# Optimization experiments

Measured on AMD Instinct MI355X. Metric: run time of the kernel, lower is better.

The kernel has to match this reference:

```python
import jax, jax.numpy as jnp
import numpy as np

N = 100000   # nodes
E = 400000   # edges
G = 2048     # graphs in batch
H = 128      # hidden_channels
V = 100      # in_channels (element vocab)
L = 3        # hidden_layers (GAT)
LO = 2       # out_layers (dense)
SLOPE = 0.2  # GATConv negative_slope default


def setup_inputs() -> dict:
    key = jax.random.key(0)
    ks = jax.random.split(key, 14)
    s = 1.0 / np.sqrt(H)
    return {
        "x": jax.random.randint(ks[0], (N,), 0, V),
        "edge_index": jax.random.randint(ks[1], (2, E), 0, N),
        "edge_attr": jax.random.uniform(ks[2], (E, 1), dtype=jnp.float32),
        "batch": jnp.sort(jax.random.randint(ks[3], (N,), 0, G)),
        "emb": jax.random.normal(ks[4], (V, H), dtype=jnp.float32),
        "gat_W": jax.random.normal(ks[5], (L, H, H), dtype=jnp.float32) * s,
        "att_src": jax.random.normal(ks[6], (L, H), dtype=jnp.float32) * s,
        "att_dst": jax.random.normal(ks[7], (L, H), dtype=jnp.float32) * s,
        "edge_W": jax.random.normal(ks[8], (L, H), dtype=jnp.float32) * s,  # lin_edge: Linear(1, H, bias=False)
        "att_edge": jax.random.normal(ks[9], (L, H), dtype=jnp.float32) * s,
        "gat_b": jnp.zeros((L, H), dtype=jnp.float32),
        "lin_W": jax.random.normal(ks[10], (LO, H, H), dtype=jnp.float32) * s,
        "lin_b": jnp.zeros((LO, H), dtype=jnp.float32),
        "wp_W": jax.random.normal(ks[11], (H, 1), dtype=jnp.float32) * s,
        "wp_b": jnp.zeros((1,), dtype=jnp.float32),
    }


def _segment_softmax(logits, seg, num_segments):
    m = jax.ops.segment_max(logits, seg, num_segments=num_segments)
    e = jnp.exp(logits - m[seg])
    s = jax.ops.segment_sum(e, seg, num_segments=num_segments)
    return e / s[seg]


def reference(x, edge_index, edge_attr, batch, emb, gat_W, att_src, att_dst,
              edge_W, att_edge, gat_b, lin_W, lin_b, wp_W, wp_b):
    src, dst = edge_index[0], edge_index[1]
    # GATConv add_self_loops=True with fill_value='mean' for edge_attr
    loop = jnp.arange(N, dtype=src.dtype)
    src_sl = jnp.concatenate([src, loop])          # [E+N]
    dst_sl = jnp.concatenate([dst, loop])          # [E+N]
    ea_mean = jnp.mean(edge_attr, axis=0, keepdims=True)  # [1,1]
    ea_sl = jnp.concatenate([edge_attr, jnp.broadcast_to(ea_mean, (N, 1))], axis=0)  # [E+N,1]

    h = emb[x]  # [N,H]
    for l in range(L):
        xt = h @ gat_W[l]                 # shared lin_src/lin_dst, heads=1
        a_s = xt @ att_src[l]             # [N]
        a_d = xt @ att_dst[l]             # [N]
        a_e = (ea_sl * edge_W[l][None, :]) @ att_edge[l]  # lin_edge then att_edge: [E+N]
        alpha = jax.nn.leaky_relu(a_s[src_sl] + a_d[dst_sl] + a_e, negative_slope=SLOPE)
        alpha = _segment_softmax(alpha, dst_sl, N)
        out = jax.ops.segment_sum(xt[src_sl] * alpha[:, None], dst_sl, num_segments=N)
        out = out + gat_b[l]
        # F.normalize(h_x, 2, dim=1)
        nrm = jnp.linalg.norm(out, axis=1, keepdims=True)
        h = out / jnp.maximum(nrm, 1e-12)
    for i in range(LO):
        h = jax.nn.relu(h @ lin_W[i] + lin_b[i])
    m_x = jax.ops.segment_sum(h, batch, num_segments=G)  # scatter_sum readout [G,H]
    props = m_x @ wp_W + wp_b                            # [G,1]
    return jnp.squeeze(props, axis=1)                    # [G]
```

## Files before the change

### kernel.cpp

```cpp
#include <hip/hip_runtime.h>
#include <math.h>

#define N_NODES 100000
#define N_EDGES 400000
#define NG 2048
#define H 128
#define NV 100
#define NLAYERS 3
#define SLOPE 0.2f

#define SCAL_N 64

typedef __attribute__((ext_vector_type(8))) short bf16x8;
typedef __attribute__((ext_vector_type(4))) float f32x4;

__device__ __forceinline__ float wave_reduce_sum(float v){
  #pragma unroll
  for (int off = 32; off > 0; off >>= 1) v += __shfl_xor(v, off, 64);
  return v;
}
__device__ __forceinline__ unsigned short rne_bf16(float f){
  unsigned int u = __float_as_uint(f);
  u += 0x7FFF + ((u >> 16) & 1);
  return (unsigned short)(u >> 16);
}
__device__ __forceinline__ unsigned int pack_bf16x2(float lo, float hi){
  return ((unsigned int)rne_bf16(hi) << 16) | rne_bf16(lo);
}

#define PB_CONVW 320
#define PB_CONVE (PB_CONVW + 50)
#define PB_OUT   (PB_CONVE + 8)
#define PB_DOTS  (PB_OUT + 1)
#define PB_EASUM (PB_DOTS + 256)
#define PB_DEG   (PB_EASUM + 1954)
__global__ __launch_bounds__(256) void k_prep(
    const float* __restrict__ gat_W, const float* __restrict__ lin_W,
    unsigned short* __restrict__ Wf,
    const float* __restrict__ emb, unsigned short* __restrict__ embb,
    const float* __restrict__ ea, const float* __restrict__ ew,
    const float* __restrict__ ae, float* __restrict__ scal,
    const float* __restrict__ wp_b, float* __restrict__ out,
    const int* __restrict__ ei, int* __restrict__ deg,
    int* __restrict__ rank)
{
  int b = blockIdx.x, tid = threadIdx.x;
  if (b < PB_CONVW){
    int i = b*256 + tid;
    int m   = i >> 14;
    int r   = i & 16383;
    int k0i = r >> 12;
    int r3  = r & 4095;
    int ct  = r3 >> 9;
    int r4  = r3 & 511;
    int lane= r4 >> 3;
    int j   = r4 & 7;
    int q = lane >> 4, ln = lane & 15;
    int k = k0i*32 + q*8 + j;
    int n = ct*16 + ln;
    const float* src = (m < 3) ? (gat_W + m*16384) : (lin_W + (m-3)*16384);
    Wf[i] = rne_bf16(src[k*H + n]);
  } else if (b < PB_CONVE){
    int i = (b - PB_CONVW)*256 + tid;
    if (i < NV*H) embb[i] = rne_bf16(emb[i]);
  } else if (b < PB_OUT){
    int g = (b - PB_CONVE)*256 + tid;
    if (g < NG) out[g] = wp_b[0];
  } else if (b < PB_DOTS){
    int l = tid >> 6, ln = tid & 63;
    if (l < NLAYERS){
      float p = ew[l*H + ln]*ae[l*H + ln] + ew[l*H + ln + 64]*ae[l*H + ln + 64];
      p = wave_reduce_sum(p);
      if (ln == 0) atomicAdd(&scal[32 + l], p);
    }
  } else if (b < PB_EASUM){
    int i = (b - PB_DOTS)*256 + tid;
    int stride = 256*256;
    float v = 0.f;
    for (; i < N_EDGES; i += stride) v += ea[i];
    v = wave_reduce_sum(v);
    if ((tid & 63) == 0) atomicAdd(&scal[0], v);
  } else {
    int i = (b - PB_EASUM)*256 + tid;
    if (i < N_EDGES + N_NODES){
      int d = (i < N_EDGES) ? ei[N_EDGES + i] : (i - N_EDGES);
      rank[i] = atomicAdd(&deg[d], 1);
    }
  }
}

__global__ __launch_bounds__(256) void k_alloc(
    const int* __restrict__ deg, int* __restrict__ row_ptr, int* __restrict__ counter){
  __shared__ int wsum[4];
  __shared__ int base;
  int n = blockIdx.x * 256 + threadIdx.x;
  int d = (n < N_NODES) ? deg[n] : 0;
  int lane = threadIdx.x & 63, wid = threadIdx.x >> 6;
  int v = d;
  #pragma unroll
  for (int off = 1; off < 64; off <<= 1){
    int u = __shfl_up(v, off, 64);
    if (lane >= off) v += u;
  }
  if (lane == 63) wsum[wid] = v;
  __syncthreads();
  if (threadIdx.x == 0){
    int t0 = wsum[0], t1 = wsum[1], t2 = wsum[2], t3 = wsum[3];
    base = atomicAdd(counter, t0 + t1 + t2 + t3);
    wsum[0] = 0; wsum[1] = t0; wsum[2] = t0 + t1; wsum[3] = t0 + t1 + t2;
  }
  __syncthreads();
  if (n < N_NODES) row_ptr[n] = base + wsum[wid] + (v - d);
}

__global__ void k_scatter(const int* __restrict__ ei, const float* __restrict__ ea,
                          const float* __restrict__ scal, const int* __restrict__ row_ptr,
                          const int* __restrict__ rank, int* __restrict__ csr_src,
                          float* __restrict__ csr_ea){
  int i = blockIdx.x * blockDim.x + threadIdx.x;
  if (i >= N_EDGES + N_NODES) return;
  int s, d; float v;
  if (i < N_EDGES){ s = ei[i]; d = ei[N_EDGES + i]; v = ea[i]; }
  else            { s = d = i - N_EDGES; v = scal[0] * (1.0f / N_EDGES); }
  int pos = row_ptr[d] + rank[i];
  csr_src[pos] = s;
  csr_ea[pos]  = v;
}

__global__ __launch_bounds__(256, 4) void k_gemm(
    const unsigned short* __restrict__ Ab, const int* __restrict__ xmap,
    const unsigned short* __restrict__ Wf,
    unsigned short* __restrict__ Cb,
    const float* __restrict__ att1, const float* __restrict__ att2,
    float* __restrict__ a_s_out, float* __restrict__ a_d_out)
{
  __shared__ unsigned short lw[16384];
  int tid  = threadIdx.x;
  int w    = tid >> 6;
  int lane = tid & 63;
  int q    = lane >> 4;
  int ln   = lane & 15;
  int waveRow = blockIdx.x*128 + w*32;

  #pragma unroll
  for (int i = 0; i < 8; ++i){
    int base = (i*256 + w*64) * 8;
    __builtin_amdgcn_global_load_lds(
        (const __attribute__((address_space(1))) unsigned int*)(Wf + base + lane*8),
        (__attribute__((address_space(3))) unsigned int*)(lw + base),
        16, 0, 0);
  }

  bf16x8 af[2][4];
  #pragma unroll
  for (int m = 0; m < 2; ++m){
    int r = waveRow + m*16 + ln;
    if (r >= N_NODES) r = N_NODES - 1;
    if (xmap) r = xmap[r];
    const unsigned short* Ar = Ab + (size_t)r*H;
    #pragma unroll
    for (int k0i = 0; k0i < 4; ++k0i)
      af[m][k0i] = *(const bf16x8*)(Ar + k0i*32 + q*8);
  }
  __syncthreads();

  f32x4 acc[2][8];
  #pragma unroll
  for (int m = 0; m < 2; ++m)
    #pragma unroll
    for (int ct = 0; ct < 8; ++ct) acc[m][ct] = (f32x4){0.f,0.f,0.f,0.f};

  #pragma unroll
  for (int k0i = 0; k0i < 4; ++k0i){
    #pragma unroll
    for (int ct = 0; ct < 8; ++ct){
      bf16x8 bw = *(const bf16x8*)(lw + k0i*4096 + ct*512 + lane*8);
      #pragma unroll
      for (int m = 0; m < 2; ++m)
        acc[m][ct] = __builtin_amdgcn_mfma_f32_16x16x32_bf16(af[m][k0i], bw, acc[m][ct], 0,0,0);
    }
  }

  float as_l[8], ad_l[8];
  #pragma unroll
  for (int ct = 0; ct < 8; ++ct){ as_l[ct] = att1[ct*16+ln]; ad_l[ct] = att2[ct*16+ln]; }
  #pragma unroll
  for (int m = 0; m < 2; ++m){
    #pragma unroll
    for (int r = 0; r < 4; ++r){
      int grow = waveRow + m*16 + q*4 + r;
      bool ok = grow < N_NODES;
      float ps = 0.f, pd = 0.f;
      #pragma unroll
      for (int ct = 0; ct < 8; ++ct){
        float v = acc[m][ct][r];
        if (ok) Cb[(size_t)grow*H + ct*16 + ln] = rne_bf16(v);
        ps += v * as_l[ct]; pd += v * ad_l[ct];
      }
      #pragma unroll
      for (int mk = 8; mk > 0; mk >>= 1){
        ps += __shfl_xor(ps, mk, 64);
        pd += __shfl_xor(pd, mk, 64);
      }
      if (ok && ln == 0){ a_s_out[grow] = ps; a_d_out[grow] = pd; }
    }
  }
}

__global__ __launch_bounds__(256, 4) void k_dense(
    const unsigned short* __restrict__ Ab,
    const unsigned short* __restrict__ Wf,
    const float* __restrict__ b1, const float* __restrict__ b2,
    const float* __restrict__ wp, const int* __restrict__ batch,
    float* __restrict__ out)
{
  __shared__ unsigned short lw[16384];
  int tid  = threadIdx.x;
  int w    = tid >> 6;
  int lane = tid & 63;
  int q    = lane >> 4;
  int ln   = lane & 15;
  int waveRow = blockIdx.x*128 + w*32;

  #pragma unroll
  for (int i = 0; i < 8; ++i){
    int base = (i*256 + w*64) * 8;
    __builtin_amdgcn_global_load_lds(
        (const __attribute__((address_space(1))) unsigned int*)(Wf + base + lane*8),
        (__attribute__((address_space(3))) unsigned int*)(lw + base),
        16, 0, 0);
  }
  bf16x8 af[2][4];
  #pragma unroll
  for (int m = 0; m < 2; ++m){
    int r = waveRow + m*16 + ln;
    if (r >= N_NODES) r = N_NODES - 1;
    const unsigned short* Ar = Ab + (size_t)r*H;
    #pragma unroll
    for (int k0i = 0; k0i < 4; ++k0i)
      af[m][k0i] = *(const bf16x8*)(Ar + k0i*32 + q*8);
  }
  __syncthreads();

  f32x4 acc[2][8];
  #pragma unroll
  for (int m = 0; m < 2; ++m)
    #pragma unroll
    for (int ct = 0; ct < 8; ++ct) acc[m][ct] = (f32x4){0.f,0.f,0.f,0.f};
  #pragma unroll
  for (int k0i = 0; k0i < 4; ++k0i){
    #pragma unroll
    for (int ct = 0; ct < 8; ++ct){
      bf16x8 bw = *(const bf16x8*)(lw + k0i*4096 + ct*512 + lane*8);
      #pragma unroll
      for (int m = 0; m < 2; ++m)
        acc[m][ct] = __builtin_amdgcn_mfma_f32_16x16x32_bf16(af[m][k0i], bw, acc[m][ct], 0,0,0);
    }
  }
  __syncthreads();

  unsigned short* lh = lw + (w << 12);
  float b1_l[8];
  #pragma unroll
  for (int ct = 0; ct < 8; ++ct) b1_l[ct] = b1[ct*16+ln];
  #pragma unroll
  for (int m = 0; m < 2; ++m){
    #pragma unroll
    for (int r = 0; r < 4; ++r){
      int lr = m*16 + q*4 + r;
      int sw = (lr & 7) << 3;
      #pragma unroll
      for (int ct = 0; ct < 8; ++ct){
        int col = ct*16 + ln;
        lh[lr*128 + (col ^ sw)] = rne_bf16(fmaxf(acc[m][ct][r] + b1_l[ct], 0.f));
      }
    }
  }
  __syncthreads();

  bf16x8 af2[2][4];
  #pragma unroll
  for (int m = 0; m < 2; ++m){
    int lr = m*16 + ln;
    int sw = (lr & 7) << 3;
    #pragma unroll
    for (int k0i = 0; k0i < 4; ++k0i)
      af2[m][k0i] = *(const bf16x8*)(lh + lr*128 + ((k0i*32 + q*8) ^ sw));
  }
  __syncthreads();

  #pragma unroll
  for (int i = 0; i < 8; ++i){
    int base = (i*256 + w*64) * 8;
    __builtin_amdgcn_global_load_lds(
        (const __attribute__((address_space(1))) unsigned int*)(Wf + 16384 + base + lane*8),
        (__attribute__((address_space(3))) unsigned int*)(lw + base),
        16, 0, 0);
  }
  __syncthreads();

  #pragma unroll
  for (int m = 0; m < 2; ++m)
    #pragma unroll
    for (int ct = 0; ct < 8; ++ct) acc[m][ct] = (f32x4){0.f,0.f,0.f,0.f};
  #pragma unroll
  for (int k0i = 0; k0i < 4; ++k0i){
    #pragma unroll
    for (int ct = 0; ct < 8; ++ct){
      bf16x8 bw = *(const bf16x8*)(lw + k0i*4096 + ct*512 + lane*8);
      #pragma unroll
      for (int m = 0; m < 2; ++m)
        acc[m][ct] = __builtin_amdgcn_mfma_f32_16x16x32_bf16(af2[m][k0i], bw, acc[m][ct], 0,0,0);
    }
  }

  float b2_l[8], wp_l[8];
  #pragma unroll
  for (int ct = 0; ct < 8; ++ct){ b2_l[ct] = b2[ct*16+ln]; wp_l[ct] = wp[ct*16+ln]; }
  #pragma unroll
  for (int m = 0; m < 2; ++m){
    #pragma unroll
    for (int r = 0; r < 4; ++r){
      int grow = waveRow + m*16 + q*4 + r;
      bool ok = grow < N_NODES;
      float ps = 0.f;
      #pragma unroll
      for (int ct = 0; ct < 8; ++ct)
        ps += fmaxf(acc[m][ct][r] + b2_l[ct], 0.f) * wp_l[ct];
      #pragma unroll
      for (int mk = 8; mk > 0; mk >>= 1) ps += __shfl_xor(ps, mk, 64);
      if (ok && ln == 0) atomicAdd(&out[batch[grow]], ps);
    }
  }
}

__global__ __launch_bounds__(256, 4) void k_aggregate(
    const uint4* __restrict__ xtb4, const float* __restrict__ a_s,
    const float* __restrict__ a_d, const int* __restrict__ csr_src,
    const float* __restrict__ csr_ea, const int* __restrict__ row_ptr,
    const int* __restrict__ deg, const float* __restrict__ scal, int l,
    const float* __restrict__ bias, uint4* __restrict__ hb4)
{
  __shared__ int   ls_s[4][4][16];
  __shared__ float ls_w[4][4][16];
  int wid  = threadIdx.x >> 6;
  int lane = threadIdx.x & 63;
  int h    = lane >> 4;
  int c    = lane & 15;
  int n    = blockIdx.x*16 + wid*4 + h;
  int beg = row_ptr[n];
  int d   = deg[n];
  float adn = a_d[n];
  float dl  = scal[32 + l];
  int v = d;
  v = max(v, __shfl_xor(v, 16, 64));
  v = max(v, __shfl_xor(v, 32, 64));
  int maxd = v;

  float4 acA = make_float4(0.f,0.f,0.f,0.f);
  float4 acB = make_float4(0.f,0.f,0.f,0.f);
  float ss = 0.f;
  for (int base = 0; base < maxd; base += 16){
    int j = base + c;
    bool vld = (j < d);
    int s = 0; float eaj = 0.f;
    if (vld){
      int e = beg + j;
      s   = csr_src[e];
      eaj = csr_ea[e];
    }
    ls_s[wid][h][c] = s;

    int cnt = (min(16, maxd - base) + 7) & ~7;

    uint4 xv[8];
    #pragma unroll
    for (int u = 0; u < 8; ++u)
      xv[u] = xtb4[(size_t)ls_s[wid][h][u]*(H/8) + c];

    float wgt = 0.f;
    if (vld){
      float lg = a_s[s] + adn + dl*eaj;
      lg = (lg > 0.f) ? lg : SLOPE*lg;
      wgt = __expf(lg);
    }
    ls_w[wid][h][c] = wgt;

    for (int j0 = 0; j0 < cnt; j0 += 8){
      if (j0){
        #pragma unroll
        for (int u = 0; u < 8; ++u)
          xv[u] = xtb4[(size_t)ls_s[wid][h][j0 + u]*(H/8) + c];
      }
      float w8[8];
      #pragma unroll
      for (int u = 0; u < 8; ++u) w8[u] = ls_w[wid][h][j0 + u];
      #pragma unroll
      for (int u = 0; u < 8; ++u){
        float wg = w8[u];
        acA.x += wg * __uint_as_float(xv[u].x << 16);
        acA.y += wg * __uint_as_float(xv[u].x & 0xFFFF0000u);
        acA.z += wg * __uint_as_float(xv[u].y << 16);
        acA.w += wg * __uint_as_float(xv[u].y & 0xFFFF0000u);
        acB.x += wg * __uint_as_float(xv[u].z << 16);
        acB.y += wg * __uint_as_float(xv[u].z & 0xFFFF0000u);
        acB.z += wg * __uint_as_float(xv[u].w << 16);
        acB.w += wg * __uint_as_float(xv[u].w & 0xFFFF0000u);
        ss    += wg;
      }
    }
  }

  float4 bvA = *(const float4*)(bias + c*8);
  float4 bvB = *(const float4*)(bias + c*8 + 4);
  float inv = 1.0f / ss;
  acA.x = acA.x*inv + bvA.x;
  acA.y = acA.y*inv + bvA.y;
  acA.z = acA.z*inv + bvA.z;
  acA.w = acA.w*inv + bvA.w;
  acB.x = acB.x*inv + bvB.x;
  acB.y = acB.y*inv + bvB.y;
  acB.z = acB.z*inv + bvB.z;
  acB.w = acB.w*inv + bvB.w;
  float sq = acA.x*acA.x + acA.y*acA.y + acA.z*acA.z + acA.w*acA.w
           + acB.x*acB.x + acB.y*acB.y + acB.z*acB.z + acB.w*acB.w;
  #pragma unroll
  for (int off = 8; off > 0; off >>= 1) sq += __shfl_xor(sq, off, 64);
  float rn = 1.0f / fmaxf(sqrtf(sq), 1e-12f);
  uint4 o;
  o.x = pack_bf16x2(acA.x*rn, acA.y*rn);
  o.y = pack_bf16x2(acA.z*rn, acA.w*rn);
  o.z = pack_bf16x2(acB.x*rn, acB.y*rn);
  o.w = pack_bf16x2(acB.z*rn, acB.w*rn);
  hb4[(size_t)n*(H/8) + c] = o;
}

extern "C" void kernel_launch(void* const* d_in, const int* in_sizes, int n_in,
                              void* d_out, int out_size, void* d_ws, size_t ws_size,
                              hipStream_t stream) {
  const int*   x          = (const int*)  d_in[0];
  const int*   edge_index = (const int*)  d_in[1];
  const float* edge_attr  = (const float*)d_in[2];
  const int*   batch      = (const int*)  d_in[3];
  const float* emb        = (const float*)d_in[4];
  const float* gat_W      = (const float*)d_in[5];
  const float* att_src    = (const float*)d_in[6];
  const float* att_dst    = (const float*)d_in[7];
  const float* edge_W     = (const float*)d_in[8];
  const float* att_edge   = (const float*)d_in[9];
  const float* gat_b      = (const float*)d_in[10];
  const float* lin_W      = (const float*)d_in[11];
  const float* lin_b      = (const float*)d_in[12];
  const float* wp_W       = (const float*)d_in[13];
  const float* wp_b       = (const float*)d_in[14];
  float* out = (float*)d_out;

  unsigned short* hb  = (unsigned short*)d_ws;
  unsigned short* xtb = hb + (size_t)N_NODES*H;
  unsigned short* Wt  = xtb + (size_t)N_NODES*H;
  unsigned short* embb= Wt + 5*16384;
  float* a_s    = (float*)(embb + NV*H);
  float* a_d    = a_s + N_NODES;
  float* csr_ea = a_d + N_NODES;
  float* scal   = csr_ea + (N_EDGES + N_NODES);
  int*   deg    = (int*)(scal + SCAL_N);
  int*   rank   = deg + N_NODES;
  int*   row_ptr= rank + (N_EDGES + N_NODES);
  int*   csr_src= row_ptr + N_NODES;

  hipMemsetAsync(scal, 0, (size_t)(SCAL_N + N_NODES) * sizeof(float), stream);

  k_prep<<<PB_DEG, 256, 0, stream>>>(
      gat_W, lin_W, Wt, emb, embb, edge_attr, edge_W, att_edge, scal,
      wp_b, out, edge_index, deg, rank);
  k_alloc<<<(N_NODES + 255)/256, 256, 0, stream>>>(deg, row_ptr, (int*)&scal[48]);
  k_scatter<<<(N_EDGES + N_NODES + 255)/256, 256, 0, stream>>>(
      edge_index, edge_attr, scal, row_ptr, rank, csr_src, csr_ea);

  const int gemm_grid = (N_NODES + 127) / 128;
  for (int l = 0; l < NLAYERS; ++l){
    k_gemm<<<gemm_grid, 256, 0, stream>>>(
        (l == 0) ? embb : hb, (l == 0) ? x : nullptr,
        Wt + (size_t)l*16384, xtb,
        att_src + l*H, att_dst + l*H, a_s, a_d);
    k_aggregate<<<(N_NODES + 15)/16, 256, 0, stream>>>(
        (const uint4*)xtb, a_s, a_d, csr_src, csr_ea, row_ptr, deg,
        scal, l, gat_b + l*H, (uint4*)hb);
  }
  k_dense<<<gemm_grid, 256, 0, stream>>>(
      hb, Wt + (size_t)3*16384, lin_b, lin_b + H, wp_W, batch, out);
}
```

Baseline: 298.5 us.

## Precompute layer-0 transform on vocab table and replace LDS staging with shuffles

Layer 0 input is emb[x], so xt = emb[x] @ W equals (emb @ W)[x]. The code now computes the transform and attention scalars once for the 100-row vocabulary inside an extra block of k_alloc, then gathers them per node in extra blocks of k_scatter, skipping the first full-size GEMM launch. The aggregate kernel also drops its shared-memory staging of source indices and weights in favour of wave shuffles, and issues both 8-edge gather batches up front. This costs more registers in aggregate and adds a gather pass that writes the full xt array.

Result: no change. 302.4 us (+1.3%).

```diff
diff --git a/kernel.cpp b/kernel.cpp
--- a/kernel.cpp
+++ b/kernel.cpp
@@ -89,46 +89,141 @@
   }
 }
 
+#define NALLOC ((N_NODES + 255)/256)
 __global__ __launch_bounds__(256) void k_alloc(
-    const int* __restrict__ deg, int* __restrict__ row_ptr, int* __restrict__ counter){
+    const int* __restrict__ deg, int* __restrict__ row_ptr, int* __restrict__ counter,
+    const unsigned short* __restrict__ embb, const unsigned short* __restrict__ Wf,
+    unsigned short* __restrict__ xt0b, const float* __restrict__ att1,
+    const float* __restrict__ att2, float* __restrict__ tabS, float* __restrict__ tabD)
+{
+  __shared__ unsigned short lw[16384];
   __shared__ int wsum[4];
-  __shared__ int base;
-  int n = blockIdx.x * 256 + threadIdx.x;
-  int d = (n < N_NODES) ? deg[n] : 0;
-  int lane = threadIdx.x & 63, wid = threadIdx.x >> 6;
-  int v = d;
-  #pragma unroll
-  for (int off = 1; off < 64; off <<= 1){
-    int u = __shfl_up(v, off, 64);
-    if (lane >= off) v += u;
-  }
-  if (lane == 63) wsum[wid] = v;
+  __shared__ int base_s;
+  if (blockIdx.x < NALLOC){
+    int n = blockIdx.x * 256 + threadIdx.x;
+    int d = (n < N_NODES) ? deg[n] : 0;
+    int lane = threadIdx.x & 63, wid = threadIdx.x >> 6;
+    int v = d;
+    #pragma unroll
+    for (int off = 1; off < 64; off <<= 1){
+      int u = __shfl_up(v, off, 64);
+      if (lane >= off) v += u;
+    }
+    if (lane == 63) wsum[wid] = v;
+    __syncthreads();
+    if (threadIdx.x == 0){
+      int t0 = wsum[0], t1 = wsum[1], t2 = wsum[2], t3 = wsum[3];
+      base_s = atomicAdd(counter, t0 + t1 + t2 + t3);
+      wsum[0] = 0; wsum[1] = t0; wsum[2] = t0 + t1; wsum[3] = t0 + t1 + t2;
+    }
+    __syncthreads();
+    if (n < N_NODES) row_ptr[n] = base_s + wsum[wid] + (v - d);
+    return;
+  }
+
+  int tid  = threadIdx.x;
+  int w    = tid >> 6;
+  int lane = tid & 63;
+  int q    = lane >> 4;
+  int ln   = lane & 15;
+  int waveRow = w*32;
+
+  #pragma unroll
+  for (int i = 0; i < 8; ++i){
+    int base = (i*256 + w*64) * 8;
+    __builtin_amdgcn_global_load_lds(
+        (const __attribute__((address_space(1))) unsigned int*)(Wf + base + lane*8),
+        (__attribute__((address_space(3))) unsigned int*)(lw + base),
+        16, 0, 0);
+  }
+  bf16x8 af[2][4];
+  #pragma unroll
+  for (int m = 0; m < 2; ++m){
+    int r = waveRow + m*16 + ln;
+    if (r >= NV) r = NV - 1;
+    const unsigned short* Ar = embb + (size_t)r*H;
+    #pragma unroll
+    for (int k0i = 0; k0i < 4; ++k0i)
+      af[m][k0i] = *(const bf16x8*)(Ar + k0i*32 + q*8);
+  }
   __syncthreads();
-  if (threadIdx.x == 0){
-    int t0 = wsum[0], t1 = wsum[1], t2 = wsum[2], t3 = wsum[3];
-    base = atomicAdd(counter, t0 + t1 + t2 + t3);
-    wsum[0] = 0; wsum[1] = t0; wsum[2] = t0 + t1; wsum[3] = t0 + t1 + t2;
-  }
-  __syncthreads();
-  if (n < N_NODES) row_ptr[n] = base + wsum[wid] + (v - d);
-}
-
+
+  f32x4 acc[2][8];
+  #pragma unroll
+  for (int m = 0; m < 2; ++m)
+    #pragma unroll
+    for (int ct = 0; ct < 8; ++ct) acc[m][ct] = (f32x4){0.f,0.f,0.f,0.f};
+  #pragma unroll
+  for (int k0i = 0; k0i < 4; ++k0i){
+    #pragma unroll
+    for (int ct = 0; ct < 8; ++ct){
+      bf16x8 bw = *(const bf16x8*)(lw + k0i*4096 + ct*512 + lane*8);
+      #pragma unroll
+      for (int m = 0; m < 2; ++m)
+        acc[m][ct] = __builtin_amdgcn_mfma_f32_16x16x32_bf16(af[m][k0i], bw, acc[m][ct], 0,0,0);
+    }
+  }
+
+  float as_l[8], ad_l[8];
+  #pragma unroll
+  for (int ct = 0; ct < 8; ++ct){ as_l[ct] = att1[ct*16+ln]; ad_l[ct] = att2[ct*16+ln]; }
+  #pragma unroll
+  for (int m = 0; m < 2; ++m){
+    #pragma unroll
+    for (int r = 0; r < 4; ++r){
+      int grow = waveRow + m*16 + q*4 + r;
+      bool ok = grow < NV;
+      float ps = 0.f, pd = 0.f;
+      #pragma unroll
+      for (int ct = 0; ct < 8; ++ct){
+        float v = acc[m][ct][r];
+        if (ok) xt0b[(size_t)grow*H + ct*16 + ln] = rne_bf16(v);
+        ps += v * as_l[ct]; pd += v * ad_l[ct];
+      }
+      #pragma unroll
+      for (int mk = 8; mk > 0; mk >>= 1){
+        ps += __shfl_xor(ps, mk, 64);
+        pd += __shfl_xor(pd, mk, 64);
+      }
+      if (ok && ln == 0){ tabS[grow] = ps; tabD[grow] = pd; }
+    }
+  }
+}
+
+#define NSCAT ((N_EDGES + N_NODES + 255)/256)
 __global__ void k_scatter(const int* __restrict__ ei, const float* __restrict__ ea,
                           const float* __restrict__ scal, const int* __restrict__ row_ptr,
                           const int* __restrict__ rank, int* __restrict__ csr_src,
-                          float* __restrict__ csr_ea){
-  int i = blockIdx.x * blockDim.x + threadIdx.x;
-  if (i >= N_EDGES + N_NODES) return;
-  int s, d; float v;
-  if (i < N_EDGES){ s = ei[i]; d = ei[N_EDGES + i]; v = ea[i]; }
-  else            { s = d = i - N_EDGES; v = scal[0] * (1.0f / N_EDGES); }
-  int pos = row_ptr[d] + rank[i];
-  csr_src[pos] = s;
-  csr_ea[pos]  = v;
+                          float* __restrict__ csr_ea,
+                          const int* __restrict__ x, const uint4* __restrict__ xt0b4,
+                          const float* __restrict__ tabS, const float* __restrict__ tabD,
+                          uint4* __restrict__ xtb4, float* __restrict__ a_s,
+                          float* __restrict__ a_d){
+  int b = blockIdx.x;
+  if (b < NSCAT){
+    int i = b * 256 + threadIdx.x;
+    if (i >= N_EDGES + N_NODES) return;
+    int s, d; float v;
+    if (i < N_EDGES){ s = ei[i]; d = ei[N_EDGES + i]; v = ea[i]; }
+    else            { s = d = i - N_EDGES; v = scal[0] * (1.0f / N_EDGES); }
+    int pos = row_ptr[d] + rank[i];
+    csr_src[pos] = s;
+    csr_ea[pos]  = v;
+    return;
+  }
+  int gb = b - NSCAT;
+  int t  = threadIdx.x;
+  int n  = gb*16 + (t >> 4);
+  int c  = t & 15;
+  if (n >= N_NODES) return;
+  int v  = x[n];
+  xtb4[(size_t)n*(H/8) + c] = xt0b4[(size_t)v*(H/8) + c];
+  if (c == 0)      a_s[n] = tabS[v];
+  else if (c == 1) a_d[n] = tabD[v];
 }
 
 __global__ __launch_bounds__(256, 4) void k_gemm(
-    const unsigned short* __restrict__ Ab, const int* __restrict__ xmap,
+    const unsigned short* __restrict__ Ab,
     const unsigned short* __restrict__ Wf,
     unsigned short* __restrict__ Cb,
     const float* __restrict__ att1, const float* __restrict__ att2,
@@ -156,7 +251,6 @@
   for (int m = 0; m < 2; ++m){
     int r = waveRow + m*16 + ln;
     if (r >= N_NODES) r = N_NODES - 1;
-    if (xmap) r = xmap[r];
     const unsigned short* Ar = Ab + (size_t)r*H;
     #pragma unroll
     for (int k0i = 0; k0i < 4; ++k0i)
@@ -341,13 +435,12 @@
     const int* __restrict__ deg, const float* __restrict__ scal, int l,
     const float* __restrict__ bias, uint4* __restrict__ hb4)
 {
-  __shared__ int   ls_s[4][4][16];
-  __shared__ float ls_w[4][4][16];
-  int wid  = threadIdx.x >> 6;
   int lane = threadIdx.x & 63;
   int h    = lane >> 4;
   int c    = lane & 15;
+  int wid  = threadIdx.x >> 6;
   int n    = blockIdx.x*16 + wid*4 + h;
+  if (n >= N_NODES) return;
   int beg = row_ptr[n];
   int d   = deg[n];
   float adn = a_d[n];
@@ -356,6 +449,7 @@
   v = max(v, __shfl_xor(v, 16, 64));
   v = max(v, __shfl_xor(v, 32, 64));
   int maxd = v;
+  int hq = h << 4;
 
   float4 acA = make_float4(0.f,0.f,0.f,0.f);
   float4 acB = make_float4(0.f,0.f,0.f,0.f);
@@ -369,14 +463,22 @@
       s   = csr_src[e];
       eaj = csr_ea[e];
     }
-    ls_s[wid][h][c] = s;
-
     int cnt = (min(16, maxd - base) + 7) & ~7;
-
-    uint4 xv[8];
-    #pragma unroll
-    for (int u = 0; u < 8; ++u)
-      xv[u] = xtb4[(size_t)ls_s[wid][h][u]*(H/8) + c];
+    bool two = (cnt > 8);
+
+    uint4 xv0[8], xv1[8];
+    #pragma unroll
+    for (int u = 0; u < 8; ++u){
+      int su = __shfl(s, hq + u, 64);
+      xv0[u] = xtb4[(size_t)su*(H/8) + c];
+    }
+    if (two){
+      #pragma unroll
+      for (int u = 0; u < 8; ++u){
+        int su = __shfl(s, hq + 8 + u, 64);
+        xv1[u] = xtb4[(size_t)su*(H/8) + c];
+      }
+    }
 
     float wgt = 0.f;
     if (vld){
@@ -384,28 +486,32 @@
       lg = (lg > 0.f) ? lg : SLOPE*lg;
       wgt = __expf(lg);
     }
-    ls_w[wid][h][c] = wgt;
-
-    for (int j0 = 0; j0 < cnt; j0 += 8){
-      if (j0){
-        #pragma unroll
-        for (int u = 0; u < 8; ++u)
-          xv[u] = xtb4[(size_t)ls_s[wid][h][j0 + u]*(H/8) + c];
-      }
-      float w8[8];
-      #pragma unroll
-      for (int u = 0; u < 8; ++u) w8[u] = ls_w[wid][h][j0 + u];
+
+    #pragma unroll
+    for (int u = 0; u < 8; ++u){
+      float wg = __shfl(wgt, hq + u, 64);
+      acA.x += wg * __uint_as_float(xv0[u].x << 16);
+      acA.y += wg * __uint_as_float(xv0[u].x & 0xFFFF0000u);
+      acA.z += wg * __uint_as_float(xv0[u].y << 16);
+      acA.w += wg * __uint_as_float(xv0[u].y & 0xFFFF0000u);
+      acB.x += wg * __uint_as_float(xv0[u].z << 16);
+      acB.y += wg * __uint_as_float(xv0[u].z & 0xFFFF0000u);
+      acB.z += wg * __uint_as_float(xv0[u].w << 16);
+      acB.w += wg * __uint_as_float(xv0[u].w & 0xFFFF0000u);
+      ss    += wg;
+    }
+    if (two){
       #pragma unroll
       for (int u = 0; u < 8; ++u){
-        float wg = w8[u];
-        acA.x += wg * __uint_as_float(xv[u].x << 16);
-        acA.y += wg * __uint_as_float(xv[u].x & 0xFFFF0000u);
-        acA.z += wg * __uint_as_float(xv[u].y << 16);
-        acA.w += wg * __uint_as_float(xv[u].y & 0xFFFF0000u);
-        acB.x += wg * __uint_as_float(xv[u].z << 16);
-        acB.y += wg * __uint_as_float(xv[u].z & 0xFFFF0000u);
-        acB.z += wg * __uint_as_float(xv[u].w << 16);
-        acB.w += wg * __uint_as_float(xv[u].w & 0xFFFF0000u);
+        float wg = __shfl(wgt, hq + 8 + u, 64);
+        acA.x += wg * __uint_as_float(xv1[u].x << 16);
+        acA.y += wg * __uint_as_float(xv1[u].x & 0xFFFF0000u);
+        acA.z += wg * __uint_as_float(xv1[u].y << 16);
+        acA.w += wg * __uint_as_float(xv1[u].y & 0xFFFF0000u);
+        acB.x += wg * __uint_as_float(xv1[u].z << 16);
+        acB.y += wg * __uint_as_float(xv1[u].z & 0xFFFF0000u);
+        acB.z += wg * __uint_as_float(xv1[u].w << 16);
+        acB.w += wg * __uint_as_float(xv1[u].w & 0xFFFF0000u);
         ss    += wg;
       }
     }
@@ -459,7 +565,10 @@
   unsigned short* xtb = hb + (size_t)N_NODES*H;
   unsigned short* Wt  = xtb + (size_t)N_NODES*H;
   unsigned short* embb= Wt + 5*16384;
-  float* a_s    = (float*)(embb + NV*H);
+  unsigned short* xt0b= embb + NV*H;
+  float* tabS   = (float*)(xt0b + NV*H);
+  float* tabD   = tabS + NV;
+  float* a_s    = tabD + NV;
   float* a_d    = a_s + N_NODES;
   float* csr_ea = a_d + N_NODES;
   float* scal   = csr_ea + (N_EDGES + N_NODES);
@@ -473,16 +582,19 @@
   k_prep<<<PB_DEG, 256, 0, stream>>>(
       gat_W, lin_W, Wt, emb, embb, edge_attr, edge_W, att_edge, scal,
       wp_b, out, edge_index, deg, rank);
-  k_alloc<<<(N_NODES + 255)/256, 256, 0, stream>>>(deg, row_ptr, (int*)&scal[48]);
-  k_scatter<<<(N_EDGES + N_NODES + 255)/256, 256, 0, stream>>>(
-      edge_index, edge_attr, scal, row_ptr, rank, csr_src, csr_ea);
+  k_alloc<<<NALLOC + 1, 256, 0, stream>>>(
+      deg, row_ptr, (int*)&scal[48],
+      embb, Wt, xt0b, att_src, att_dst, tabS, tabD);
+  k_scatter<<<NSCAT + (N_NODES/16), 256, 0, stream>>>(
+      edge_index, edge_attr, scal, row_ptr, rank, csr_src, csr_ea,
+      x, (const uint4*)xt0b, tabS, tabD, (uint4*)xtb, a_s, a_d);
 
   const int gemm_grid = (N_NODES + 127) / 128;
   for (int l = 0; l < NLAYERS; ++l){
-    k_gemm<<<gemm_grid, 256, 0, stream>>>(
-        (l == 0) ? embb : hb, (l == 0) ? x : nullptr,
-        Wt + (size_t)l*16384, xtb,
-        att_src + l*H, att_dst + l*H, a_s, a_d);
+    if (l > 0)
+      k_gemm<<<gemm_grid, 256, 0, stream>>>(
+          hb, Wt + (size_t)l*16384, xtb,
+          att_src + l*H, att_dst + l*H, a_s, a_d);
     k_aggregate<<<(N_NODES + 15)/16, 256, 0, stream>>>(
         (const uint4*)xtb, a_s, a_d, csr_src, csr_ea, row_ptr, deg,
         scal, l, gat_b + l*H, (uint4*)hb);
```
